# Performance work log

Measured on AMD Instinct MI355X. Metric: run time of the kernel, lower is better.

## Reference

```python
import jax, jax.numpy as jnp
import numpy as np

IN = 1    # input feature dim (hardcoded in NN)
H = 10    # LSTM hidden size (hardcoded in NN)
B = 8192  # batch
T = 256   # sequence length


def setup_inputs() -> dict:
    key = jax.random.key(0)
    ks = jax.random.split(key, 12)
    s = 0.1  # init scale for mus (mimics blitz posterior_mu_init spread)
    RHO0 = -3.0  # posterior_rho_init from the module
    return {
        "x": jax.random.normal(ks[0], (B, T, IN), jnp.float32),
        # BayesianLSTM variational parameters (blitz layout: (in, 4*H), (H, 4*H), (4*H,))
        "w_ih_mu": jax.random.normal(ks[1], (IN, 4 * H), jnp.float32) * s,
        "w_ih_rho": jnp.full((IN, 4 * H), RHO0, jnp.float32),
        "w_hh_mu": jax.random.normal(ks[2], (H, 4 * H), jnp.float32) * s,
        "w_hh_rho": jnp.full((H, 4 * H), RHO0, jnp.float32),
        "b_mu": jax.random.normal(ks[3], (4 * H,), jnp.float32) * s,
        "b_rho": jnp.full((4 * H,), RHO0, jnp.float32),
        # reparameterization noise, sampled once per forward call in blitz
        "eps_ih": jax.random.normal(ks[4], (IN, 4 * H), jnp.float32),
        "eps_hh": jax.random.normal(ks[5], (H, 4 * H), jnp.float32),
        "eps_b": jax.random.normal(ks[6], (4 * H,), jnp.float32),
        # deterministic linear head nn.Linear(10, 1)
        "lin_w": jax.random.normal(ks[7], (1, H), jnp.float32) * s,
        "lin_b": jnp.zeros((1,), jnp.float32),
    }


def reference(x, w_ih_mu, w_ih_rho, w_hh_mu, w_hh_rho, b_mu, b_rho,
              eps_ih, eps_hh, eps_b, lin_w, lin_b):
    sp = jax.nn.softplus
    # sample weights: w = mu + log1p(exp(rho)) * eps
    w_ih = w_ih_mu + sp(w_ih_rho) * eps_ih   # (IN, 4H)
    w_hh = w_hh_mu + sp(w_hh_rho) * eps_hh   # (H, 4H)
    b = b_mu + sp(b_rho) * eps_b             # (4H,)

    # precompute input contribution for all timesteps: (B, T, 4H)
    x_proj = jnp.einsum('bti,ig->btg', x, w_ih) + b

    def step(carry, xg):
        h, c = carry                      # (B, H) each
        gates = xg + h @ w_hh             # (B, 4H)
        i = jax.nn.sigmoid(gates[:, :H])
        f = jax.nn.sigmoid(gates[:, H:2 * H])
        g = jnp.tanh(gates[:, 2 * H:3 * H])
        o = jax.nn.sigmoid(gates[:, 3 * H:])
        c = f * c + i * g
        h = o * jnp.tanh(c)
        return (h, c), None

    h0 = jnp.zeros((x.shape[0], H), x.dtype)
    (h_last, _), _ = jax.lax.scan(step, (h0, h0), jnp.swapaxes(x_proj, 0, 1))
    # NN takes hidden_seq[:, -1, :] == final hidden state, then linear head
    return h_last @ lin_w.T + lin_b  # (B, 1)
```

## Files before the change

### kernel.cpp

```cpp
#include <hip/hip_runtime.h>
#include <math.h>

#define T_LEN 256
#define HID 10

typedef float v2f __attribute__((ext_vector_type(2)));

__device__ __forceinline__ v2f mk2(float a, float b) { v2f r; r.x = a; r.y = b; return r; }

template <int PAT>
__device__ __forceinline__ float swz(float v) {
    return __int_as_float(__builtin_amdgcn_ds_swizzle(__float_as_int(v), PAT));
}

__device__ __forceinline__ float softplus_f(float x) {
    return fmaxf(x, 0.0f) + log1pf(expf(-fabsf(x)));
}
__device__ __forceinline__ float samp(const float* mu, const float* rho,
                                      const float* eps, int i) {
    return mu[i] + softplus_f(rho[i]) * eps[i];
}

__device__ __forceinline__ float fast_sigmoid(float x) {
    float e = __builtin_amdgcn_exp2f(-1.442695040888963f * x);
    return __builtin_amdgcn_rcpf(1.0f + e);
}
__device__ __forceinline__ float fast_tanh(float x) {
    float e = __builtin_amdgcn_exp2f(2.885390081777927f * x);
    return fmaf(-2.0f, __builtin_amdgcn_rcpf(e + 1.0f), 1.0f);
}

#define GATE_J(J)                                                        \
    {                                                                    \
        float hj = swz<((J) << 5) | 0x10>(hk);                           \
        v2f hj2 = mk2(hj, hj);                                           \
        if ((J) % 2 == 0) {                                              \
            a01 = __builtin_elementwise_fma(hj2, whh01[J], a01);         \
            a23 = __builtin_elementwise_fma(hj2, whh23[J], a23);         \
        } else {                                                         \
            a01o = __builtin_elementwise_fma(hj2, whh01[J], a01o);       \
            a23o = __builtin_elementwise_fma(hj2, whh23[J], a23o);       \
        }                                                                \
    }

#define TSTEP(TI)                                                        \
    {                                                                    \
        float xt = swz<((TI) << 5) | 0x10>(xcur);                        \
        v2f xt2 = mk2(xt, xt);                                           \
        v2f a01 = __builtin_elementwise_fma(xt2, wih01, b01);            \
        v2f a23 = __builtin_elementwise_fma(xt2, wih23, b23);            \
        v2f a01o = mk2(0.f, 0.f), a23o = mk2(0.f, 0.f);                  \
        GATE_J(0) GATE_J(1) GATE_J(2) GATE_J(3) GATE_J(4)                \
        GATE_J(5) GATE_J(6) GATE_J(7) GATE_J(8) GATE_J(9)                \
        a01 = a01 + a01o;                                                \
        a23 = a23 + a23o;                                                \
        float ig = fast_sigmoid(a01.x);                                  \
        float fg = fast_sigmoid(a01.y);                                  \
        float gg = fast_tanh(a23.x);                                     \
        float og = fast_sigmoid(a23.y);                                  \
        c = fmaf(fg, c, ig * gg);                                        \
        hk = og * fast_tanh(c);                                          \
    }

__global__ __launch_bounds__(256) void bayes_lstm_kernel(
    const float* __restrict__ x,
    const float* __restrict__ w_ih_mu, const float* __restrict__ w_ih_rho,
    const float* __restrict__ w_hh_mu, const float* __restrict__ w_hh_rho,
    const float* __restrict__ b_mu,    const float* __restrict__ b_rho,
    const float* __restrict__ eps_ih,  const float* __restrict__ eps_hh,
    const float* __restrict__ eps_b,
    const float* __restrict__ lin_w,   const float* __restrict__ lin_b,
    float* __restrict__ out)
{
    const int tid   = threadIdx.x;
    const int k     = tid & 15;
    const int group = tid >> 4;
    const int b     = blockIdx.x * 16 + group;

    v2f whh01[HID], whh23[HID];
    v2f wih01 = mk2(0.f, 0.f), wih23 = mk2(0.f, 0.f);
    v2f b01   = mk2(0.f, 0.f), b23   = mk2(0.f, 0.f);
#pragma unroll
    for (int j = 0; j < HID; ++j) { whh01[j] = mk2(0.f, 0.f); whh23[j] = mk2(0.f, 0.f); }

    float lw = 0.f;
    if (k < HID) {
        const int c0 = k, c1 = HID + k, c2 = 2 * HID + k, c3 = 3 * HID + k;
        wih01 = mk2(samp(w_ih_mu, w_ih_rho, eps_ih, c0), samp(w_ih_mu, w_ih_rho, eps_ih, c1));
        wih23 = mk2(samp(w_ih_mu, w_ih_rho, eps_ih, c2), samp(w_ih_mu, w_ih_rho, eps_ih, c3));
        b01   = mk2(samp(b_mu, b_rho, eps_b, c0), samp(b_mu, b_rho, eps_b, c1));
        b23   = mk2(samp(b_mu, b_rho, eps_b, c2), samp(b_mu, b_rho, eps_b, c3));
#pragma unroll
        for (int j = 0; j < HID; ++j) {
            whh01[j] = mk2(samp(w_hh_mu, w_hh_rho, eps_hh, j * 4 * HID + c0),
                           samp(w_hh_mu, w_hh_rho, eps_hh, j * 4 * HID + c1));
            whh23[j] = mk2(samp(w_hh_mu, w_hh_rho, eps_hh, j * 4 * HID + c2),
                           samp(w_hh_mu, w_hh_rho, eps_hh, j * 4 * HID + c3));
        }
        lw = lin_w[k];
    }

    float hk = 0.0f;
    float c  = 0.0f;

    const float* xrow = x + (size_t)b * T_LEN;
    float xcur = xrow[k];

    for (int to = 0; to < 16; ++to) {
        float xnext = 0.0f;
        if (to < 15) xnext = xrow[(to + 1) * 16 + k];
        TSTEP(0)  TSTEP(1)  TSTEP(2)  TSTEP(3)
        TSTEP(4)  TSTEP(5)  TSTEP(6)  TSTEP(7)
        TSTEP(8)  TSTEP(9)  TSTEP(10) TSTEP(11)
        TSTEP(12) TSTEP(13) TSTEP(14) TSTEP(15)
        xcur = xnext;
    }

    float part = hk * lw;
    part += swz<(1 << 10) | 0x1f>(part);
    part += swz<(2 << 10) | 0x1f>(part);
    part += swz<(4 << 10) | 0x1f>(part);
    part += swz<(8 << 10) | 0x1f>(part);
    if (k == 0) out[b] = part + lin_b[0];
}

extern "C" void kernel_launch(void* const* d_in, const int* in_sizes, int n_in,
                              void* d_out, int out_size, void* d_ws, size_t ws_size,
                              hipStream_t stream) {
    const float* x        = (const float*)d_in[0];
    const float* w_ih_mu  = (const float*)d_in[1];
    const float* w_ih_rho = (const float*)d_in[2];
    const float* w_hh_mu  = (const float*)d_in[3];
    const float* w_hh_rho = (const float*)d_in[4];
    const float* b_mu     = (const float*)d_in[5];
    const float* b_rho    = (const float*)d_in[6];
    const float* eps_ih   = (const float*)d_in[7];
    const float* eps_hh   = (const float*)d_in[8];
    const float* eps_b    = (const float*)d_in[9];
    const float* lin_w    = (const float*)d_in[10];
    const float* lin_b    = (const float*)d_in[11];
    float* out = (float*)d_out;

    const int n_b = in_sizes[0] / T_LEN;
    dim3 grid(n_b / 16), block(256);
    hipLaunchKernelGGL(bayes_lstm_kernel, grid, block, 0, stream,
                       x, w_ih_mu, w_ih_rho, w_hh_mu, w_hh_rho, b_mu, b_rho,
                       eps_ih, eps_hh, eps_b, lin_w, lin_b, out);
}
```

Before: 168.3 us.

## Broadcast hidden state via LDS and interleave two batch rows per lane group

Each 16-lane group now runs two independent batch sequences at once, giving two interleaved dependency chains per timestep. The hidden state is shared through LDS: each lane writes its h and reads the full vector back with vector loads, replacing the ten per-step ds_swizzle broadcasts. Packed v2f FMAs become scalar FMAs, the final reduction uses shfl_xor, and the grid is halved. In exchange the kernel issues more FMA instructions, runs fewer waves per CU, and relies on in-wave LDS ordering with no explicit barrier.

```diff
diff --git a/kernel.cpp b/kernel.cpp
--- a/kernel.cpp
+++ b/kernel.cpp
@@ -3,10 +3,6 @@
 
 #define T_LEN 256
 #define HID 10
-
-typedef float v2f __attribute__((ext_vector_type(2)));
-
-__device__ __forceinline__ v2f mk2(float a, float b) { v2f r; r.x = a; r.y = b; return r; }
 
 template <int PAT>
 __device__ __forceinline__ float swz(float v) {
@@ -30,36 +26,45 @@
     return fmaf(-2.0f, __builtin_amdgcn_rcpf(e + 1.0f), 1.0f);
 }
 
-#define GATE_J(J)                                                        \
+#define GATES(HV, XT, CC, HK)                                            \
     {                                                                    \
-        float hj = swz<((J) << 5) | 0x10>(hk);                           \
-        v2f hj2 = mk2(hj, hj);                                           \
-        if ((J) % 2 == 0) {                                              \
-            a01 = __builtin_elementwise_fma(hj2, whh01[J], a01);         \
-            a23 = __builtin_elementwise_fma(hj2, whh23[J], a23);         \
-        } else {                                                         \
-            a01o = __builtin_elementwise_fma(hj2, whh01[J], a01o);       \
-            a23o = __builtin_elementwise_fma(hj2, whh23[J], a23o);       \
+        float gi = fmaf((XT), wih[0], bs[0]);                            \
+        float gf = fmaf((XT), wih[1], bs[1]);                            \
+        float gg = fmaf((XT), wih[2], bs[2]);                            \
+        float go = fmaf((XT), wih[3], bs[3]);                            \
+        _Pragma("unroll")                                                \
+        for (int j = 0; j < HID; ++j) {                                  \
+            gi = fmaf(HV[j], whi[j], gi);                                \
+            gf = fmaf(HV[j], whf[j], gf);                                \
+            gg = fmaf(HV[j], whg[j], gg);                                \
+            go = fmaf(HV[j], who[j], go);                                \
         }                                                                \
+        float si = fast_sigmoid(gi);                                     \
+        float sf = fast_sigmoid(gf);                                     \
+        float tg = fast_tanh(gg);                                        \
+        float so = fast_sigmoid(go);                                     \
+        (CC) = fmaf(sf, (CC), si * tg);                                  \
+        (HK) = so * fast_tanh(CC);                                       \
     }
 
 #define TSTEP(TI)                                                        \
     {                                                                    \
-        float xt = swz<((TI) << 5) | 0x10>(xcur);                        \
-        v2f xt2 = mk2(xt, xt);                                           \
-        v2f a01 = __builtin_elementwise_fma(xt2, wih01, b01);            \
-        v2f a23 = __builtin_elementwise_fma(xt2, wih23, b23);            \
-        v2f a01o = mk2(0.f, 0.f), a23o = mk2(0.f, 0.f);                  \
-        GATE_J(0) GATE_J(1) GATE_J(2) GATE_J(3) GATE_J(4)                \
-        GATE_J(5) GATE_J(6) GATE_J(7) GATE_J(8) GATE_J(9)                \
-        a01 = a01 + a01o;                                                \
-        a23 = a23 + a23o;                                                \
-        float ig = fast_sigmoid(a01.x);                                  \
-        float fg = fast_sigmoid(a01.y);                                  \
-        float gg = fast_tanh(a23.x);                                     \
-        float og = fast_sigmoid(a23.y);                                  \
-        c = fmaf(fg, c, ig * gg);                                        \
-        hk = og * fast_tanh(c);                                          \
+        float4 hA0 = *(const float4*)(hbA);                              \
+        float4 hA1 = *(const float4*)(hbA + 4);                          \
+        float2 hA2 = *(const float2*)(hbA + 8);                          \
+        float4 hB0 = *(const float4*)(hbB);                              \
+        float4 hB1 = *(const float4*)(hbB + 4);                          \
+        float2 hB2 = *(const float2*)(hbB + 8);                          \
+        float xa = swz<((TI) << 5) | 0x10>(xcA);                         \
+        float xb = swz<((TI) << 5) | 0x10>(xcB);                         \
+        float hvA[HID] = {hA0.x, hA0.y, hA0.z, hA0.w,                    \
+                          hA1.x, hA1.y, hA1.z, hA1.w, hA2.x, hA2.y};     \
+        float hvB[HID] = {hB0.x, hB0.y, hB0.z, hB0.w,                    \
+                          hB1.x, hB1.y, hB1.z, hB1.w, hB2.x, hB2.y};     \
+        GATES(hvA, xa, cA, hkA);                                         \
+        GATES(hvB, xb, cB, hkB);                                         \
+        wrA[0] = hkA;                                                    \
+        wrB[0] = hkB;                                                    \
     }
 
 __global__ __launch_bounds__(256) void bayes_lstm_kernel(
@@ -72,56 +77,79 @@
     const float* __restrict__ lin_w,   const float* __restrict__ lin_b,
     float* __restrict__ out)
 {
-    const int tid   = threadIdx.x;
-    const int k     = tid & 15;
-    const int group = tid >> 4;
-    const int b     = blockIdx.x * 16 + group;
+    __shared__ __align__(16) float hbuf[16 * 2 * 20];
 
-    v2f whh01[HID], whh23[HID];
-    v2f wih01 = mk2(0.f, 0.f), wih23 = mk2(0.f, 0.f);
-    v2f b01   = mk2(0.f, 0.f), b23   = mk2(0.f, 0.f);
+    const int tid  = threadIdx.x;
+    const int k    = tid & 15;
+    const int slot = tid >> 4;
+    const int bA   = (blockIdx.x * 16 + slot) * 2;
+    const int bB   = bA + 1;
+
+    float* hbA = hbuf + (slot * 2 + 0) * 20;
+    float* hbB = hbuf + (slot * 2 + 1) * 20;
+    float* wrA = hbA + k;
+    float* wrB = hbB + k;
+
+    float whi[HID], whf[HID], whg[HID], who[HID];
+    float wih[4] = {0.f, 0.f, 0.f, 0.f};
+    float bs[4]  = {0.f, 0.f, 0.f, 0.f};
+    float lw = 0.f;
 #pragma unroll
-    for (int j = 0; j < HID; ++j) { whh01[j] = mk2(0.f, 0.f); whh23[j] = mk2(0.f, 0.f); }
+    for (int j = 0; j < HID; ++j) { whi[j] = 0.f; whf[j] = 0.f; whg[j] = 0.f; who[j] = 0.f; }
 
-    float lw = 0.f;
     if (k < HID) {
         const int c0 = k, c1 = HID + k, c2 = 2 * HID + k, c3 = 3 * HID + k;
-        wih01 = mk2(samp(w_ih_mu, w_ih_rho, eps_ih, c0), samp(w_ih_mu, w_ih_rho, eps_ih, c1));
-        wih23 = mk2(samp(w_ih_mu, w_ih_rho, eps_ih, c2), samp(w_ih_mu, w_ih_rho, eps_ih, c3));
-        b01   = mk2(samp(b_mu, b_rho, eps_b, c0), samp(b_mu, b_rho, eps_b, c1));
-        b23   = mk2(samp(b_mu, b_rho, eps_b, c2), samp(b_mu, b_rho, eps_b, c3));
+        wih[0] = samp(w_ih_mu, w_ih_rho, eps_ih, c0);
+        wih[1] = samp(w_ih_mu, w_ih_rho, eps_ih, c1);
+        wih[2] = samp(w_ih_mu, w_ih_rho, eps_ih, c2);
+        wih[3] = samp(w_ih_mu, w_ih_rho, eps_ih, c3);
+        bs[0]  = samp(b_mu, b_rho, eps_b, c0);
+        bs[1]  = samp(b_mu, b_rho, eps_b, c1);
+        bs[2]  = samp(b_mu, b_rho, eps_b, c2);
+        bs[3]  = samp(b_mu, b_rho, eps_b, c3);
 #pragma unroll
         for (int j = 0; j < HID; ++j) {
-            whh01[j] = mk2(samp(w_hh_mu, w_hh_rho, eps_hh, j * 4 * HID + c0),
-                           samp(w_hh_mu, w_hh_rho, eps_hh, j * 4 * HID + c1));
-            whh23[j] = mk2(samp(w_hh_mu, w_hh_rho, eps_hh, j * 4 * HID + c2),
-                           samp(w_hh_mu, w_hh_rho, eps_hh, j * 4 * HID + c3));
+            whi[j] = samp(w_hh_mu, w_hh_rho, eps_hh, j * 4 * HID + c0);
+            whf[j] = samp(w_hh_mu, w_hh_rho, eps_hh, j * 4 * HID + c1);
+            whg[j] = samp(w_hh_mu, w_hh_rho, eps_hh, j * 4 * HID + c2);
+            who[j] = samp(w_hh_mu, w_hh_rho, eps_hh, j * 4 * HID + c3);
         }
         lw = lin_w[k];
     }
 
-    float hk = 0.0f;
-    float c  = 0.0f;
+    wrA[0] = 0.f;
+    wrB[0] = 0.f;
 
-    const float* xrow = x + (size_t)b * T_LEN;
-    float xcur = xrow[k];
+    float cA = 0.f, cB = 0.f, hkA = 0.f, hkB = 0.f;
+    const float* xrA = x + (size_t)bA * T_LEN;
+    const float* xrB = x + (size_t)bB * T_LEN;
+    float xcA = xrA[k];
+    float xcB = xrB[k];
 
     for (int to = 0; to < 16; ++to) {
-        float xnext = 0.0f;
-        if (to < 15) xnext = xrow[(to + 1) * 16 + k];
+        float xnA = 0.f, xnB = 0.f;
+        if (to < 15) {
+            xnA = xrA[(to + 1) * 16 + k];
+            xnB = xrB[(to + 1) * 16 + k];
+        }
         TSTEP(0)  TSTEP(1)  TSTEP(2)  TSTEP(3)
         TSTEP(4)  TSTEP(5)  TSTEP(6)  TSTEP(7)
         TSTEP(8)  TSTEP(9)  TSTEP(10) TSTEP(11)
         TSTEP(12) TSTEP(13) TSTEP(14) TSTEP(15)
-        xcur = xnext;
+        xcA = xnA; xcB = xnB;
     }
 
-    float part = hk * lw;
-    part += swz<(1 << 10) | 0x1f>(part);
-    part += swz<(2 << 10) | 0x1f>(part);
-    part += swz<(4 << 10) | 0x1f>(part);
-    part += swz<(8 << 10) | 0x1f>(part);
-    if (k == 0) out[b] = part + lin_b[0];
+    float pa = hkA * lw;
+    float pb = hkB * lw;
+    pa += __shfl_xor(pa, 1, 16);  pb += __shfl_xor(pb, 1, 16);
+    pa += __shfl_xor(pa, 2, 16);  pb += __shfl_xor(pb, 2, 16);
+    pa += __shfl_xor(pa, 4, 16);  pb += __shfl_xor(pb, 4, 16);
+    pa += __shfl_xor(pa, 8, 16);  pb += __shfl_xor(pb, 8, 16);
+    if (k == 0) {
+        float b0 = lin_b[0];
+        out[bA] = pa + b0;
+        out[bB] = pb + b0;
+    }
 }
 
 extern "C" void kernel_launch(void* const* d_in, const int* in_sizes, int n_in,
@@ -142,7 +170,7 @@
     float* out = (float*)d_out;
 
     const int n_b = in_sizes[0] / T_LEN;
-    dim3 grid(n_b / 16), block(256);
+    dim3 grid(n_b / 32), block(256);
     hipLaunchKernelGGL(bayes_lstm_kernel, grid, block, 0, stream,
                        x, w_ih_mu, w_ih_rho, w_hh_mu, w_hh_rho, b_mu, b_rho,
                        eps_ih, eps_hh, eps_b, lin_w, lin_b, out);
```

After: 177.2 us. 5.3% more time.
